# Kernel tuning notes

Measured on AMD Instinct MI355X. Metric: run time of the kernel, lower is better.

The kernel has to match this reference:

```python
import jax, jax.numpy as jnp
import numpy as np

N_NODES = 8      # 4 regions + 4 boundaries
N_STEPS = 3


def _step_graph(nodes, Wd, Ws, b):
    """One all-pairs message-passing step.

    nodes: [N, B, C, H, W]
    Wd:    [N, C, C]  receiver-i conv weight acting on (nodes[j] - nodes[i])
    Ws:    [N, C, C]  receiver-i conv weight acting on nodes[i]
    b:     [N, C]
    edges[j][i] = Wd_i @ (nodes[j]-nodes[i]) + Ws_i @ nodes[i] + b_i   (1x1 conv)
    out[i] = sum_{j != i} relu(edges[j][i]) * nodes[j] + nodes[i]
    """
    # receiver-dependent self term: [N(i), B, C, H, W]
    self_term = jnp.einsum('iod,ibdhw->ibohw', Ws, nodes) + b[:, None, :, None, None]
    # pairwise differences nodes[j] - nodes[i]: [N(j), N(i), B, C, H, W]
    diff = nodes[:, None] - nodes[None, :]
    e = jnp.einsum('iod,jibdhw->jibohw', Wd, diff) + self_term[None]
    gate = jax.nn.relu(e)
    # zero out the diagonal (i == j contributes nothing)
    mask = (1.0 - jnp.eye(N_NODES, dtype=nodes.dtype))[:, :, None, None, None, None]
    gate = gate * mask
    # message[i] = sum_j gate[j,i] * nodes[j]
    msg = jnp.einsum('jibchw,jbchw->ibchw', gate, nodes)
    return msg + nodes


def setup_inputs() -> dict:
    key = jax.random.key(0)
    k1, k2, k3 = jax.random.split(key, 3)
    B, C, H, W = 4, 32, 96, 96
    nodes = jax.random.normal(k1, (N_NODES, B, C, H, W), dtype=jnp.float32)
    # 1x1 conv weights [N, C_out, 2C_in]; scaled ~1/(2C) to keep 3 steps numerically tame
    W_edge = jax.random.normal(k2, (N_NODES, C, 2 * C), dtype=jnp.float32) * 0.05
    b_edge = jax.random.normal(k3, (N_NODES, C), dtype=jnp.float32) * 0.05
    return {"nodes": nodes, "W_edge": W_edge, "b_edge": b_edge}


def reference(nodes, W_edge, b_edge):
    C = nodes.shape[2]
    Wd = W_edge[:, :, :C]   # acts on nodes[j] - nodes[i]
    Ws = W_edge[:, :, C:]   # acts on nodes[i]
    for _ in range(N_STEPS):
        nodes = _step_graph(nodes, Wd, Ws, b_edge)
    return nodes  # [N, B, C, H, W]; first half = regions, second half = boundaries
```

## Files before the change

kernel.cpp:

```cpp
#include <hip/hip_runtime.h>
#include <hip/hip_bf16.h>


#define NN 8
#define NSTEPS 3
#define BB 4
#define CC 32
#define HWSZ 9216
#define PX 16
#define CPS 40
#define CPG 36
#define MSC 2048.0f
#define SINV 4.8828125e-4f

typedef _Float16 f16x8 __attribute__((ext_vector_type(8)));
typedef _Float16 f16x4 __attribute__((ext_vector_type(4)));
typedef _Float16 f16x2 __attribute__((ext_vector_type(2)));
typedef float    f32x4 __attribute__((ext_vector_type(4)));
typedef float    f32x2 __attribute__((ext_vector_type(2)));

#define MFMA(A, B, C) __builtin_amdgcn_mfma_f32_16x16x32_f16((A), (B), (C), 0, 0, 0)

__device__ __forceinline__ void split2s(float v, _Float16& h, _Float16& m) {
    h = (_Float16)v;
    m = (_Float16)((v - (float)h) * MSC);
}

__global__ __launch_bounds__(512, 4)
void gcn3_f16w(const float* __restrict__ nodes,
               const float* __restrict__ we,
               const float* __restrict__ be,
               float* __restrict__ out) {
    __shared__ _Float16 xs[2][NN][PX][CPS];
    __shared__ float    xg[NN][PX][CPG];

    const int tid  = threadIdx.x;
    const int wid  = tid >> 6;
    const int lane = tid & 63;
    const int col  = lane & 15;
    const int quad = lane >> 4;

    const f32x4 zero4 = {0.f, 0.f, 0.f, 0.f};

    f16x8 awd[2][2], awsd[2][2];
    f32x4 bias[2];
    #pragma unroll
    for (int t = 0; t < 2; ++t) {
        const float* wp = we + (size_t)((wid * CC + 16 * t + col) * (2 * CC)) + quad * 8;
        f32x4 d0 = *(const f32x4*)wp;
        f32x4 d1 = *(const f32x4*)(wp + 4);
        f32x4 s0 = *(const f32x4*)(wp + CC);
        f32x4 s1 = *(const f32x4*)(wp + CC + 4);
        #pragma unroll
        for (int k = 0; k < 8; ++k) {
            float d = (k < 4) ? d0[k & 3] : d1[k & 3];
            float s = (k < 4) ? s0[k & 3] : s1[k & 3];
            _Float16 h, m;
            split2s(d, h, m);
            awd[t][0][k] = h; awd[t][1][k] = m;
            split2s(s - d, h, m);
            awsd[t][0][k] = h; awsd[t][1][k] = m;
        }
        #pragma unroll
        for (int k = 0; k < 4; ++k)
            bias[t][k] = be[wid * CC + 16 * t + quad * 4 + k];
    }

    const int q0  = blockIdx.x * PX;
    const int b   = q0 / HWSZ;
    const int hw0 = q0 - b * HWSZ;

    #pragma unroll
    for (int kk = 0; kk < 2; ++kk) {
        int idx = tid + kk * 512;
        int p2 = (idx & 7) * 2;
        int c2 = ((idx >> 3) & 15) * 2;
        int n  = idx >> 7;
        const float* gp = nodes + (size_t)((n * BB + b) * CC + c2) * HWSZ + hw0 + p2;
        f32x2 v0 = *(const f32x2*)gp;
        f32x2 v1 = *(const f32x2*)(gp + HWSZ);
        #pragma unroll
        for (int e = 0; e < 2; ++e) {
            _Float16 h0, m0, h1, m1;
            split2s(v0[e], h0, m0);
            split2s(v1[e], h1, m1);
            *(f16x2*)&xs[0][n][p2 + e][c2] = f16x2{h0, h1};
            *(f16x2*)&xs[1][n][p2 + e][c2] = f16x2{m0, m1};
            *(f32x2*)&xg[n][p2 + e][c2] = f32x2{v0[e], v1[e]};
        }
    }
    __syncthreads();

    f32x4 msg[2];

    #pragma unroll 1
    for (int step = 0; step < NSTEPS; ++step) {
        f32x4 qf[2];
        {
            f16x8 bh = *(const f16x8*)&xs[0][wid][col][quad * 8];
            f16x8 bm = *(const f16x8*)&xs[1][wid][col][quad * 8];
            #pragma unroll
            for (int t = 0; t < 2; ++t) {
                f32x4 q1 = MFMA(awsd[t][0], bh, bias[t]);
                f32x4 q2 = MFMA(awsd[t][0], bm, zero4);
                q2 = MFMA(awsd[t][1], bh, q2);
                f32x4 q3 = MFMA(awsd[t][1], bm, zero4);
                #pragma unroll
                for (int k = 0; k < 4; ++k)
                    qf[t][k] = fmaf(fmaf(q3[k], SINV, q2[k]), SINV, q1[k]);
            }
        }

        #pragma unroll
        for (int t = 0; t < 2; ++t)
            msg[t] = zero4;

        #pragma unroll
        for (int j = 0; j < NN; ++j) {
            f32x4 xgj[2];
            #pragma unroll
            for (int t = 0; t < 2; ++t)
                xgj[t] = *(const f32x4*)&xg[j][col][16 * t + quad * 4];
            if (j == wid) {
                #pragma unroll
                for (int t = 0; t < 2; ++t)
                    #pragma unroll
                    for (int k = 0; k < 4; ++k)
                        msg[t][k] += xgj[t][k];
            } else {
                f16x8 bh = *(const f16x8*)&xs[0][j][col][quad * 8];
                f16x8 bm = *(const f16x8*)&xs[1][j][col][quad * 8];
                #pragma unroll
                for (int t = 0; t < 2; ++t) {
                    f32x4 e1 = MFMA(awd[t][0], bh, qf[t]);
                    f32x4 e2 = MFMA(awd[t][0], bm, zero4);
                    e2 = MFMA(awd[t][1], bh, e2);
                    #pragma unroll
                    for (int k = 0; k < 4; ++k) {
                        float g = fmaxf(fmaf(e2[k], SINV, e1[k]), 0.f);
                        msg[t][k] = fmaf(g, xgj[t][k], msg[t][k]);
                    }
                }
            }
        }

        if (step < NSTEPS - 1) {
            __syncthreads();
            #pragma unroll
            for (int t = 0; t < 2; ++t) {
                f16x4 h4, m4;
                #pragma unroll
                for (int k = 0; k < 4; ++k) {
                    _Float16 h, m;
                    split2s(msg[t][k], h, m);
                    h4[k] = h; m4[k] = m;
                }
                *(f16x4*)&xs[0][wid][col][16 * t + quad * 4] = h4;
                *(f16x4*)&xs[1][wid][col][16 * t + quad * 4] = m4;
                *(f32x4*)&xg[wid][col][16 * t + quad * 4] = msg[t];
            }
            __syncthreads();
        }
    }

    __syncthreads();
    #pragma unroll
    for (int t = 0; t < 2; ++t)
        *(f32x4*)&xg[wid][col][16 * t + quad * 4] = msg[t];
    __syncthreads();
    #pragma unroll
    for (int kk = 0; kk < 2; ++kk) {
        int idx = tid + kk * 512;
        int p4 = (idx & 3) * 4;
        int c  = (idx >> 2) & 31;
        int n  = idx >> 7;
        f32x4 v;
        #pragma unroll
        for (int e = 0; e < 4; ++e) v[e] = xg[n][p4 + e][c];
        *(f32x4*)(out + (size_t)((n * BB + b) * CC + c) * HWSZ + hw0 + p4) = v;
    }
}

extern "C" void kernel_launch(void* const* d_in, const int* in_sizes, int n_in,
                              void* d_out, int out_size, void* d_ws, size_t ws_size,
                              hipStream_t stream) {
    const float* nodes  = (const float*)d_in[0];
    const float* W_edge = (const float*)d_in[1];
    const float* b_edge = (const float*)d_in[2];
    float* outp = (float*)d_out;

    dim3 grid((BB * HWSZ) / PX);
    dim3 block(512);
    gcn3_f16w<<<grid, block, 0, stream>>>(nodes, W_edge, b_edge, outp);
}
```

Before: 133.5 us.

## Store LDS tiles in MFMA fragment order and write output directly from registers

The shared-memory tiles are reorganised so each lane's MFMA B-operand and gate values sit at a contiguous lane-indexed slot, replacing padded strided layouts. This aims to remove bank conflicts and address arithmetic on the hot per-j reads. The epilogue drops the LDS transpose and two barriers and stores results straight from registers. Those stores are scalar, 16 consecutive floats per row (64B segments), which may coalesce less well than the earlier f32x4 stores.

```diff
diff --git a/kernel.cpp b/kernel.cpp
--- a/kernel.cpp
+++ b/kernel.cpp
@@ -8,8 +8,6 @@
 #define CC 32
 #define HWSZ 9216
 #define PX 16
-#define CPS 40
-#define CPG 36
 #define MSC 2048.0f
 #define SINV 4.8828125e-4f
 
@@ -31,8 +29,8 @@
                const float* __restrict__ we,
                const float* __restrict__ be,
                float* __restrict__ out) {
-    __shared__ _Float16 xs[2][NN][PX][CPS];
-    __shared__ float    xg[NN][PX][CPG];
+    __shared__ _Float16 xsf[2][NN][64][8];
+    __shared__ float    xgf[NN][2][64][4];
 
     const int tid  = threadIdx.x;
     const int wid  = tid >> 6;
@@ -81,12 +79,13 @@
         f32x2 v1 = *(const f32x2*)(gp + HWSZ);
         #pragma unroll
         for (int e = 0; e < 2; ++e) {
+            int px = p2 + e;
             _Float16 h0, m0, h1, m1;
             split2s(v0[e], h0, m0);
             split2s(v1[e], h1, m1);
-            *(f16x2*)&xs[0][n][p2 + e][c2] = f16x2{h0, h1};
-            *(f16x2*)&xs[1][n][p2 + e][c2] = f16x2{m0, m1};
-            *(f32x2*)&xg[n][p2 + e][c2] = f32x2{v0[e], v1[e]};
+            *(f16x2*)&xsf[0][n][(c2 >> 3) * 16 + px][c2 & 7] = f16x2{h0, h1};
+            *(f16x2*)&xsf[1][n][(c2 >> 3) * 16 + px][c2 & 7] = f16x2{m0, m1};
+            *(f32x2*)&xgf[n][c2 >> 4][((c2 >> 2) & 3) * 16 + px][c2 & 3] = f32x2{v0[e], v1[e]};
         }
     }
     __syncthreads();
@@ -97,8 +96,8 @@
     for (int step = 0; step < NSTEPS; ++step) {
         f32x4 qf[2];
         {
-            f16x8 bh = *(const f16x8*)&xs[0][wid][col][quad * 8];
-            f16x8 bm = *(const f16x8*)&xs[1][wid][col][quad * 8];
+            f16x8 bh = *(const f16x8*)&xsf[0][wid][lane][0];
+            f16x8 bm = *(const f16x8*)&xsf[1][wid][lane][0];
             #pragma unroll
             for (int t = 0; t < 2; ++t) {
                 f32x4 q1 = MFMA(awsd[t][0], bh, bias[t]);
@@ -120,7 +119,7 @@
             f32x4 xgj[2];
             #pragma unroll
             for (int t = 0; t < 2; ++t)
-                xgj[t] = *(const f32x4*)&xg[j][col][16 * t + quad * 4];
+                xgj[t] = *(const f32x4*)&xgf[j][t][lane][0];
             if (j == wid) {
                 #pragma unroll
                 for (int t = 0; t < 2; ++t)
@@ -128,8 +127,8 @@
                     for (int k = 0; k < 4; ++k)
                         msg[t][k] += xgj[t][k];
             } else {
-                f16x8 bh = *(const f16x8*)&xs[0][j][col][quad * 8];
-                f16x8 bm = *(const f16x8*)&xs[1][j][col][quad * 8];
+                f16x8 bh = *(const f16x8*)&xsf[0][j][lane][0];
+                f16x8 bm = *(const f16x8*)&xsf[1][j][lane][0];
                 #pragma unroll
                 for (int t = 0; t < 2; ++t) {
                     f32x4 e1 = MFMA(awd[t][0], bh, qf[t]);
@@ -155,30 +154,21 @@
                     split2s(msg[t][k], h, m);
                     h4[k] = h; m4[k] = m;
                 }
-                *(f16x4*)&xs[0][wid][col][16 * t + quad * 4] = h4;
-                *(f16x4*)&xs[1][wid][col][16 * t + quad * 4] = m4;
-                *(f32x4*)&xg[wid][col][16 * t + quad * 4] = msg[t];
+                int lane2 = (2 * t + (quad >> 1)) * 16 + col;
+                int e0    = (quad & 1) * 4;
+                *(f16x4*)&xsf[0][wid][lane2][e0] = h4;
+                *(f16x4*)&xsf[1][wid][lane2][e0] = m4;
+                *(f32x4*)&xgf[wid][t][lane][0] = msg[t];
             }
             __syncthreads();
         }
     }
 
-    __syncthreads();
     #pragma unroll
     for (int t = 0; t < 2; ++t)
-        *(f32x4*)&xg[wid][col][16 * t + quad * 4] = msg[t];
-    __syncthreads();
-    #pragma unroll
-    for (int kk = 0; kk < 2; ++kk) {
-        int idx = tid + kk * 512;
-        int p4 = (idx & 3) * 4;
-        int c  = (idx >> 2) & 31;
-        int n  = idx >> 7;
-        f32x4 v;
         #pragma unroll
-        for (int e = 0; e < 4; ++e) v[e] = xg[n][p4 + e][c];
-        *(f32x4*)(out + (size_t)((n * BB + b) * CC + c) * HWSZ + hw0 + p4) = v;
-    }
+        for (int k = 0; k < 4; ++k)
+            out[(size_t)((wid * BB + b) * CC + 16 * t + quad * 4 + k) * HWSZ + hw0 + col] = msg[t][k];
 }
 
 extern "C" void kernel_launch(void* const* d_in, const int* in_sizes, int n_in,
```

Result: no change. 132.9 us (-0.4%).
